# Kernel tuning notes

Measured on AMD Instinct MI355X. Metric: run time of the kernel, lower is better.

The kernel has to match this reference:

```python
import jax, jax.numpy as jnp
import numpy as np

NEG_BIG = -9.0e15  # matches torch's -9000000000000000.0
LEAKY_SLOPE = 0.01  # nn.LeakyReLU default


def setup_inputs() -> dict:
    key = jax.random.key(0)
    k1, k2, k3, k4, k5, k6 = jax.random.split(key, 6)
    B, N, NEMB, NHID = 1, 8192, 128, 64
    x = jax.random.normal(k1, (B, N, NEMB), dtype=jnp.float32)
    adj = jax.random.randint(k2, (B, N, N), 0, 2, dtype=jnp.int32)
    # learned parameters (xavier-ish scale)
    w_weight = jax.random.normal(k3, (NHID, NEMB), dtype=jnp.float32) * (1.0 / np.sqrt(NEMB))
    w_bias = jnp.zeros((NHID,), dtype=jnp.float32)
    a_weight = jax.random.normal(k4, (1, 2 * NHID), dtype=jnp.float32) * (1.0 / np.sqrt(2 * NHID))
    a_bias = jnp.zeros((1,), dtype=jnp.float32)
    return {"x": x, "adj": adj, "w_weight": w_weight, "w_bias": w_bias,
            "a_weight": a_weight, "a_bias": a_bias}


def reference(x, adj, w_weight, w_bias, a_weight, a_bias):
    # h = W x + b : [B, N, F]
    h = jnp.einsum("bnd,fd->bnf", x, w_weight) + w_bias
    F = h.shape[-1]
    # The torch code forms a[b,i,j] = concat(h_i, h_j) then Linear(2F->1).
    # Equivalent decomposition avoids the [B,N,N,2F] tensor:
    # e[b,i,j] = leaky_relu(h_i . a_src + h_j . a_dst + a_bias)
    a_src, a_dst = a_weight[0, :F], a_weight[0, F:]
    s_src = jnp.einsum("bnf,f->bn", h, a_src)  # [B, N]
    s_dst = jnp.einsum("bnf,f->bn", h, a_dst)  # [B, N]
    e = jax.nn.leaky_relu(s_src[:, :, None] + s_dst[:, None, :] + a_bias[0],
                          negative_slope=LEAKY_SLOPE)  # [B, N, N]
    # masked_scatter_ semantics: True positions (row-major over the WHOLE
    # flattened tensor) receive e's elements taken sequentially in order.
    mask_flat = (adj > 0).reshape(-1)
    take_idx = jnp.cumsum(mask_flat.astype(jnp.int32)) - 1  # position in source stream
    src_flat = e.reshape(-1)
    att = jnp.where(mask_flat, src_flat[take_idx], jnp.float32(NEG_BIG)).reshape(e.shape)
    # softmax over dim=2, dropout in eval mode (identity)
    att = jax.nn.softmax(att, axis=2)
    out = jax.nn.elu(jnp.einsum("bij,bjf->bif", att, h))  # [B, N, F]
    return out
```

## Files before the change

kernel.cpp:

```cpp
#include <hip/hip_runtime.h>
#include <cstdint>
#include <cstddef>

#define N 8192
#define F 64
#define NEMB 128
#define BI 16
#define BJ 256
#define NCHUNK 32
#define HALFCH 16
#define ROWSTR 560
#define LEAKY 0.01f
#define LOG2E 1.44269504f

typedef __attribute__((ext_vector_type(8))) short bf16x8;
typedef __attribute__((ext_vector_type(4))) float f32x4;

__device__ __forceinline__ float wave_reduce_sum_f(float v){
  #pragma unroll
  for (int d = 32; d > 0; d >>= 1) v += __shfl_xor(v, d, 64);
  return v;
}
__device__ __forceinline__ int wave_reduce_sum_i(int v){
  #pragma unroll
  for (int d = 32; d > 0; d >>= 1) v += __shfl_xor(v, d, 64);
  return v;
}
__device__ __forceinline__ int wave_incl_scan_i(int v, int lane){
  #pragma unroll
  for (int d = 1; d < 64; d <<= 1){
    int u = __shfl_up(v, d, 64);
    if (lane >= d) v += u;
  }
  return v;
}
__device__ __forceinline__ unsigned short f2bf(float x){
  union { float f; unsigned u; } v; v.f = x;
  unsigned r = v.u + 0x7fff + ((v.u >> 16) & 1);
  return (unsigned short)(r >> 16);
}

extern "C" __global__ void __launch_bounds__(256)
k_packh(const int* __restrict__ adj, unsigned short* __restrict__ bm,
        unsigned short* __restrict__ ccnt, int* __restrict__ rowtot,
        const float* __restrict__ x, const float* __restrict__ ww,
        const float* __restrict__ wb, const float* __restrict__ aw,
        const float* __restrict__ abias,
        float* __restrict__ h, float* __restrict__ ssrc, float* __restrict__ sdst2x){
  const int t = threadIdx.x;
  if (blockIdx.x < N){
    const int i = blockIdx.x;
    int total = 0;
    #pragma unroll
    for (int half = 0; half < 2; ++half){
      const int w = half*256 + t;
      const int4* p4 = (const int4*)(adj + (size_t)i*N + w*16);
      unsigned m = 0;
      #pragma unroll
      for (int k = 0; k < 4; ++k){
        int4 a = p4[k];
        m |= (unsigned)(a.x>0) << (k*4+0);
        m |= (unsigned)(a.y>0) << (k*4+1);
        m |= (unsigned)(a.z>0) << (k*4+2);
        m |= (unsigned)(a.w>0) << (k*4+3);
      }
      bm[((size_t)(i >> 4)*NCHUNK + (w >> 4))*256 + (i & 15)*16 + (w & 15)] =
          (unsigned short)m;
      const int pc = __popc(m);
      total += pc;
      int cs = pc;
      cs += __shfl_xor(cs, 1, 16);
      cs += __shfl_xor(cs, 2, 16);
      cs += __shfl_xor(cs, 4, 16);
      cs += __shfl_xor(cs, 8, 16);
      if ((t & 15) == 0) ccnt[(size_t)i*NCHUNK + (w>>4)] = (unsigned short)cs;
    }
    total = wave_reduce_sum_i(total);
    __shared__ int ws_[4];
    if ((t & 63) == 0) ws_[t >> 6] = total;
    __syncthreads();
    if (t == 0) rowtot[i] = ws_[0] + ws_[1] + ws_[2] + ws_[3];
  } else {
    const int w = t >> 6, lane = t & 63;
    __shared__ float xs[4][NEMB];
    const int n0 = (blockIdx.x - N) * 4;
    ((float2*)&xs[0][0])[t] = ((const float2*)(x + (size_t)n0 * NEMB))[t];
    __syncthreads();
    const int n = n0 + w;
    const float4* w4 = (const float4*)(ww + (size_t)lane * NEMB);
    const float4* x4 = (const float4*)&xs[w][0];
    float acc = wb[lane];
    #pragma unroll
    for (int k = 0; k < NEMB/4; ++k){
      float4 a = x4[k]; float4 b = w4[k];
      acc = fmaf(a.x, b.x, acc);
      acc = fmaf(a.y, b.y, acc);
      acc = fmaf(a.z, b.z, acc);
      acc = fmaf(a.w, b.w, acc);
    }
    h[(size_t)n * F + lane] = acc;
    float vs = wave_reduce_sum_f(acc * aw[lane]);
    float vd = wave_reduce_sum_f(acc * aw[F + lane]);
    if (lane == 0){
      ssrc[n] = (vs + abias[0]) * LOG2E;
      const float vdl = vd * LOG2E;
      sdst2x[n] = vdl; sdst2x[n + N] = vdl;
    }
  }
}

extern "C" __global__ void __launch_bounds__(256)
k_tr(const float* __restrict__ h, unsigned short* __restrict__ ht){
  __shared__ float tile[64][65];
  const int t = threadIdx.x;
  const int n0 = blockIdx.x * 64;
  #pragma unroll
  for (int s = 0; s < 4; ++s){
    const int r = s*16 + (t>>4);
    const int c = (t&15)*4;
    const float4 v = *(const float4*)(h + (size_t)(n0+r)*F + c);
    tile[r][c] = v.x; tile[r][c+1] = v.y; tile[r][c+2] = v.z; tile[r][c+3] = v.w;
  }
  __syncthreads();
  const int f = t >> 2, jq = t & 3;
  unsigned short buf[16];
  #pragma unroll
  for (int k = 0; k < 16; ++k) buf[k] = f2bf(tile[jq*16 + k][f]);
  *(uint4*)(ht + (size_t)f*N + n0 + jq*16)     = *(uint4*)&buf[0];
  *(uint4*)(ht + (size_t)f*N + n0 + jq*16 + 8) = *(uint4*)&buf[8];
}

extern "C" __global__ void __launch_bounds__(1024)
k_scan(const int* __restrict__ cnt, int* __restrict__ base){
  __shared__ int wsum[16];
  const int t = threadIdx.x, lane = t & 63, w = t >> 6;
  int4 aa = ((const int4*)cnt)[t * 2];
  int4 bb = ((const int4*)cnt)[t * 2 + 1];
  int v[8] = {aa.x, aa.y, aa.z, aa.w, bb.x, bb.y, bb.z, bb.w};
  int local = 0;
  #pragma unroll
  for (int k = 0; k < 8; ++k){ int tmp = v[k]; v[k] = local; local += tmp; }
  int inc = wave_incl_scan_i(local, lane);
  int wexcl = inc - local;
  if (lane == 63) wsum[w] = inc;
  __syncthreads();
  if (t == 0){
    int run = 0;
    #pragma unroll
    for (int k = 0; k < 16; ++k){ int tmp = wsum[k]; wsum[k] = run; run += tmp; }
  }
  __syncthreads();
  const int b0 = wsum[w] + wexcl;
  ((int4*)base)[t * 2]     = make_int4(b0 + v[0], b0 + v[1], b0 + v[2], b0 + v[3]);
  ((int4*)base)[t * 2 + 1] = make_int4(b0 + v[4], b0 + v[5], b0 + v[6], b0 + v[7]);
}

extern "C" __global__ void __launch_bounds__(256, 4)
k_main(const unsigned short* __restrict__ bm, const unsigned short* __restrict__ ccnt,
       const int* __restrict__ base, const unsigned short* __restrict__ ht,
       const float* __restrict__ ssrc, const float* __restrict__ sdst2x,
       float* __restrict__ pnum, float* __restrict__ pden){
  __shared__ __attribute__((aligned(16))) char pt[2][16*ROWSTR];
  __shared__ unsigned short ccum[BI][HALFCH];
  __shared__ int basel[BI];

  const int t = threadIdx.x, w = t >> 6, lane = t & 63;
  const int vid = blockIdx.x >> 1, half = blockIdx.x & 1;
  const int i0 = vid * BI;
  const int ch0 = half * HALFCH;

  if (t < BI) basel[t] = base[i0 + t];
  const int r = t >> 4, g = t & 15;
  {
    int c = (int)ccnt[(size_t)(i0+r)*NCHUNK + ch0 + g];
    int pre = 0;
    if (half){
      pre = (int)ccnt[(size_t)(i0+r)*NCHUNK + g];
      #pragma unroll
      for (int d = 1; d < 16; d <<= 1) pre += __shfl_xor(pre, d, 16);
    }
    int inc = c;
    #pragma unroll
    for (int d = 1; d < 16; d <<= 1){ int u = __shfl_up(inc, d, 16); if (g >= d) inc += u; }
    ccum[r][g] = (unsigned short)(pre + inc - c);
  }
  __syncthreads();

  const int fr = lane & 15, ks = lane >> 4;
  const int fB = w*16 + fr;
  char* buf0 = pt[0];
  char* buf1 = pt[1];
  const int rowbase = basel[r];
  float dsum = 0.f;
  f32x4 acc = {0.f, 0.f, 0.f, 0.f};
  bf16x8 bregA[8], bregB[8];

#define BMLD(CC) ((unsigned)bm[((size_t)vid*NCHUNK + ch0 + (CC))*256 + t])

#define PREFETCH(CH, BR) { \
    const unsigned short* hBp = ht + (size_t)fB*N + (CH)*BJ + ks*8; \
    _Pragma("unroll") \
    for (int kk = 0; kk < 8; ++kk) BR[kk] = *(const bf16x8*)(hBp + kk*32); \
    __builtin_amdgcn_sched_barrier(0); \
  }

#define PRODUCE(CC, PB, MV) { \
    const unsigned m = (MV); \
    const unsigned mlo = m & 0xffu, mhi = m >> 8; \
    const int clo = __popc(mlo), chi = __popc(mhi); \
    const int c = clo + chi; \
    int inc = c; \
    _Pragma("unroll") \
    for (int d = 1; d < 16; d <<= 1){ int u = __shfl_up(inc, d, 16); if (g >= d) inc += u; } \
    const int qex = inc - c; \
    const int q0row = rowbase + (int)ccum[r][CC]; \
    const float* sdw = sdst2x + (q0row & (N - 1)) + qex; \
    const int ilo = q0row >> 13; \
    const float s_lo = ssrc[ilo]; \
    const float s_hi = ssrc[ilo + 1]; \
    const int krel = ((ilo + 1) << 13) - q0row - qex; \
    char* myrow = (PB) + r*ROWSTR; \
    *(uint4*)(myrow + g*32)      = make_uint4(0,0,0,0); \
    *(uint4*)(myrow + g*32 + 16) = make_uint4(0,0,0,0); \
    float wvlo[8], wvhi[8]; \
    const float* sdh = sdw + clo; \
    _Pragma("unroll") \
    for (int k = 0; k < 8; ++k){ wvlo[k] = sdw[k]; wvhi[k] = sdh[k]; } \
    float dlo = 0.f, dhi = 0.f; \
    unsigned mcl = mlo, mch = mhi; \
    _Pragma("unroll") \
    for (int k = 0; k < 8; ++k){ \
      { \
        const float ss = (k >= krel) ? s_hi : s_lo; \
        float e = ss + wvlo[k]; \
        e = fmaxf(e, LEAKY * e); \
        float p; \
        asm("v_exp_f32 %0, %1" : "=v"(p) : "v"(e)); \
        const int pos = __ffs(mcl) - 1; \
        const bool act = (k < clo); \
        dlo += act ? p : 0.f; \
        const int off = act ? (g*32 + pos*2) : (512 + g*2); \
        *(unsigned short*)(myrow + off) = \
            (unsigned short)((__float_as_uint(p) + 0x8000u) >> 16); \
        mcl &= mcl - 1; \
      } \
      { \
        const int kg = clo + k; \
        const float ss = (kg >= krel) ? s_hi : s_lo; \
        float e = ss + wvhi[k]; \
        e = fmaxf(e, LEAKY * e); \
        float p; \
        asm("v_exp_f32 %0, %1" : "=v"(p) : "v"(e)); \
        const int pos = __ffs(mch) + 7; \
        const bool act = (k < chi); \
        dhi += act ? p : 0.f; \
        const int off = act ? (g*32 + pos*2) : (512 + g*2); \
        *(unsigned short*)(myrow + off) = \
            (unsigned short)((__float_as_uint(p) + 0x8000u) >> 16); \
        mch &= mch - 1; \
      } \
    } \
    dsum += dlo + dhi; \
  }

#define MM(PB, BR) { \
    const char* aP = (PB) + fr*ROWSTR; \
    __builtin_amdgcn_s_setprio(1); \
    _Pragma("unroll") \
    for (int kk = 0; kk < 8; ++kk){ \
      bf16x8 av = *(const bf16x8*)(aP + kk*64 + ks*16); \
      acc = __builtin_amdgcn_mfma_f32_16x16x32_bf16(av, BR[kk], acc, 0, 0, 0); \
    } \
    __builtin_amdgcn_s_setprio(0); \
  }

  unsigned mCur = BMLD(0);
  unsigned mNxt = BMLD(1);
  PREFETCH(ch0, bregA)
  PRODUCE(0, buf0, mCur)
  __syncthreads();
  for (int cc = 0; cc < HALFCH; cc += 2){
    {
      PREFETCH(ch0 + cc + 1, bregB)
      const unsigned mUse = mNxt;
      if (cc + 2 < HALFCH) mNxt = BMLD(cc + 2);
      PRODUCE(cc + 1, buf1, mUse)
      MM(buf0, bregA)
    }
    __syncthreads();
    if (cc + 2 < HALFCH){
      PREFETCH(ch0 + cc + 2, bregA)
      const unsigned mUse = mNxt;
      if (cc + 3 < HALFCH) mNxt = BMLD(cc + 3);
      PRODUCE(cc + 2, buf0, mUse)
      MM(buf1, bregB)
    } else {
      MM(buf1, bregB)
    }
    __syncthreads();
  }
#undef BMLD
#undef PREFETCH
#undef PRODUCE
#undef MM

  #pragma unroll
  for (int d = 8; d > 0; d >>= 1) dsum += __shfl_xor(dsum, d, 16);
  if (g == 0) pden[(size_t)half*N + i0 + r] = dsum;
  #pragma unroll
  for (int reg = 0; reg < 4; ++reg){
    const int il = ks*4 + reg;
    pnum[(size_t)half*N*F + (size_t)(i0 + il)*F + fB] = acc[reg];
  }
}

extern "C" __global__ void __launch_bounds__(256)
k_comb(const float* __restrict__ pnum, const float* __restrict__ pden,
       float* __restrict__ out){
  const int idx = blockIdx.x * 256 + threadIdx.x;
  const int i = idx >> 6;
  const float dn = pden[i] + pden[N + i];
  const float nm = pnum[idx] + pnum[(size_t)N*F + idx];
  float v = (dn > 0.f) ? nm / dn : 0.f;
  out[idx] = (v > 0.f) ? v : (__expf(v) - 1.f);
}

extern "C" void kernel_launch(void* const* d_in, const int* in_sizes, int n_in,
                              void* d_out, int out_size, void* d_ws, size_t ws_size,
                              hipStream_t stream){
  const float* x   = (const float*)d_in[0];
  const int*   adj = (const int*)d_in[1];
  const float* ww  = (const float*)d_in[2];
  const float* wb  = (const float*)d_in[3];
  const float* aw  = (const float*)d_in[4];
  const float* ab  = (const float*)d_in[5];
  float* out = (float*)d_out;

  char* ws = (char*)d_ws;
  float*          h      = (float*)(ws);
  unsigned short* ht     = (unsigned short*)(ws + (2u<<20));
  float*          ssrc   = (float*)(ws + (3u<<20));
  float*          sdst2x = (float*)(ws + (3u<<20) + 32*1024);
  int*            rowtot = (int*)(ws + (3u<<20) + 96*1024);
  int*            base   = (int*)(ws + (3u<<20) + 128*1024);
  unsigned short* ccnt   = (unsigned short*)(ws + (3u<<20) + 160*1024);
  unsigned short* bm     = (unsigned short*)(ws + (4u<<20));
  float*          pnum   = (float*)(ws + (12u<<20));
  float*          pden   = (float*)(ws + (16u<<20));

  k_packh<<<N + N/4, 256, 0, stream>>>(adj, bm, ccnt, rowtot,
                                       x, ww, wb, aw, ab, h, ssrc, sdst2x);
  k_tr  <<<N/64,   256, 0, stream>>>(h, ht);
  k_scan<<<1,     1024, 0, stream>>>(rowtot, base);
  k_main<<<2*(N/BI), 256, 0, stream>>>(bm, ccnt, base, ht, ssrc, sdst2x, pnum, pden);
  k_comb<<<(N*F)/256, 256, 0, stream>>>(pnum, pden, out);
}
```

Measured before the change: 160.5 us.

## Double column chunk width to 512 with 32-bit mask packing and single B register set

```diff
diff --git a/kernel.cpp b/kernel.cpp
--- a/kernel.cpp
+++ b/kernel.cpp
@@ -6,10 +6,10 @@
 #define F 64
 #define NEMB 128
 #define BI 16
-#define BJ 256
-#define NCHUNK 32
-#define HALFCH 16
-#define ROWSTR 560
+#define BJ 512
+#define NCH2 16
+#define HALFCH 8
+#define ROWSTR 1072
 #define LEAKY 0.01f
 #define LOG2E 1.44269504f
 
@@ -41,7 +41,7 @@
 }
 
 extern "C" __global__ void __launch_bounds__(256)
-k_packh(const int* __restrict__ adj, unsigned short* __restrict__ bm,
+k_packh(const int* __restrict__ adj, unsigned* __restrict__ bm32,
         unsigned short* __restrict__ ccnt, int* __restrict__ rowtot,
         const float* __restrict__ x, const float* __restrict__ ww,
         const float* __restrict__ wb, const float* __restrict__ aw,
@@ -64,16 +64,21 @@
         m |= (unsigned)(a.z>0) << (k*4+2);
         m |= (unsigned)(a.w>0) << (k*4+3);
       }
-      bm[((size_t)(i >> 4)*NCHUNK + (w >> 4))*256 + (i & 15)*16 + (w & 15)] =
-          (unsigned short)m;
+      const unsigned mo = (unsigned)__shfl_xor((int)m, 1, 64);
+      if ((t & 1) == 0){
+        const int w32 = w >> 1;
+        const int ch = w32 >> 4, gg = w32 & 15;
+        bm32[((size_t)(i >> 4)*NCH2 + ch)*256 + (i & 15)*16 + gg] = m | (mo << 16);
+      }
       const int pc = __popc(m);
       total += pc;
       int cs = pc;
-      cs += __shfl_xor(cs, 1, 16);
-      cs += __shfl_xor(cs, 2, 16);
-      cs += __shfl_xor(cs, 4, 16);
-      cs += __shfl_xor(cs, 8, 16);
-      if ((t & 15) == 0) ccnt[(size_t)i*NCHUNK + (w>>4)] = (unsigned short)cs;
+      cs += __shfl_xor(cs, 1, 32);
+      cs += __shfl_xor(cs, 2, 32);
+      cs += __shfl_xor(cs, 4, 32);
+      cs += __shfl_xor(cs, 8, 32);
+      cs += __shfl_xor(cs, 16, 32);
+      if ((t & 31) == 0) ccnt[(size_t)i*NCH2 + half*8 + (t>>5)] = (unsigned short)cs;
     }
     total = wave_reduce_sum_i(total);
     __shared__ int ws_[4];
@@ -156,7 +161,7 @@
 }
 
 extern "C" __global__ void __launch_bounds__(256, 4)
-k_main(const unsigned short* __restrict__ bm, const unsigned short* __restrict__ ccnt,
+k_main(const unsigned* __restrict__ bm32, const unsigned short* __restrict__ ccnt,
        const int* __restrict__ base, const unsigned short* __restrict__ ht,
        const float* __restrict__ ssrc, const float* __restrict__ sdst2x,
        float* __restrict__ pnum, float* __restrict__ pden){
@@ -172,17 +177,15 @@
   if (t < BI) basel[t] = base[i0 + t];
   const int r = t >> 4, g = t & 15;
   {
-    int c = (int)ccnt[(size_t)(i0+r)*NCHUNK + ch0 + g];
-    int pre = 0;
-    if (half){
-      pre = (int)ccnt[(size_t)(i0+r)*NCHUNK + g];
-      #pragma unroll
-      for (int d = 1; d < 16; d <<= 1) pre += __shfl_xor(pre, d, 16);
-    }
+    const unsigned short* cr = ccnt + (size_t)(i0+r)*NCH2;
+    int pre = (g < ch0) ? (int)cr[g] : 0;
+    #pragma unroll
+    for (int d = 1; d < 16; d <<= 1) pre += __shfl_xor(pre, d, 16);
+    int c = (g < HALFCH) ? (int)cr[ch0 + g] : 0;
     int inc = c;
     #pragma unroll
     for (int d = 1; d < 16; d <<= 1){ int u = __shfl_up(inc, d, 16); if (g >= d) inc += u; }
-    ccum[r][g] = (unsigned short)(pre + inc - c);
+    if (g < HALFCH) ccum[r][g] = (unsigned short)(pre + inc - c);
   }
   __syncthreads();
 
@@ -193,26 +196,47 @@
   const int rowbase = basel[r];
   float dsum = 0.f;
   f32x4 acc = {0.f, 0.f, 0.f, 0.f};
-  bf16x8 bregA[8], bregB[8];
-
-#define BMLD(CC) ((unsigned)bm[((size_t)vid*NCHUNK + ch0 + (CC))*256 + t])
-
-#define PREFETCH(CH, BR) { \
+  bf16x8 breg[16];
+
+#define BMLD(CC) (bm32[((size_t)vid*NCH2 + ch0 + (CC))*256 + t])
+
+#define PREFETCH(CH) { \
     const unsigned short* hBp = ht + (size_t)fB*N + (CH)*BJ + ks*8; \
     _Pragma("unroll") \
-    for (int kk = 0; kk < 8; ++kk) BR[kk] = *(const bf16x8*)(hBp + kk*32); \
+    for (int kk = 0; kk < 16; ++kk) breg[kk] = *(const bf16x8*)(hBp + kk*32); \
     __builtin_amdgcn_sched_barrier(0); \
   }
 
-#define PRODUCE(CC, PB, MV) { \
-    const unsigned m = (MV); \
-    const unsigned mlo = m & 0xffu, mhi = m >> 8; \
-    const int clo = __popc(mlo), chi = __popc(mhi); \
-    const int c = clo + chi; \
-    int inc = c; \
+#define CHAIN(MASK, CNT, WV, EOFF, BYOFF, DACC) \
+    { \
+      unsigned mc = (MASK); \
+      _Pragma("unroll") \
+      for (int k = 0; k < 8; ++k){ \
+        const int e = (EOFF) + k; \
+        const float ss = (e >= krel) ? s_hi : s_lo; \
+        float ev = ss + (WV)[k]; \
+        ev = fmaxf(ev, LEAKY * ev); \
+        float p; \
+        asm("v_exp_f32 %0, %1" : "=v"(p) : "v"(ev)); \
+        const int pos = __ffs(mc) - 1; \
+        const bool act = (k < (CNT)); \
+        DACC += act ? p : 0.f; \
+        const int off = act ? ((BYOFF) + pos*2) : (1024 + g*2); \
+        *(unsigned short*)(myrow + off) = \
+            (unsigned short)((__float_as_uint(p) + 0x8000u) >> 16); \
+        mc &= mc - 1; \
+      } \
+    }
+
+#define PRODUCE(CC, PB, UV) { \
+    const unsigned u_ = (UV); \
+    const unsigned mA = u_ & 0xffffu, mB = u_ >> 16; \
+    const int cA = __popc(mA), cB = __popc(mB); \
+    const int ct = cA + cB; \
+    int inc = ct; \
     _Pragma("unroll") \
-    for (int d = 1; d < 16; d <<= 1){ int u = __shfl_up(inc, d, 16); if (g >= d) inc += u; } \
-    const int qex = inc - c; \
+    for (int d = 1; d < 16; d <<= 1){ int uu = __shfl_up(inc, d, 16); if (g >= d) inc += uu; } \
+    const int qex = inc - ct; \
     const int q0row = rowbase + (int)ccum[r][CC]; \
     const float* sdw = sdst2x + (q0row & (N - 1)) + qex; \
     const int ilo = q0row >> 13; \
@@ -220,87 +244,65 @@
     const float s_hi = ssrc[ilo + 1]; \
     const int krel = ((ilo + 1) << 13) - q0row - qex; \
     char* myrow = (PB) + r*ROWSTR; \
-    *(uint4*)(myrow + g*32)      = make_uint4(0,0,0,0); \
-    *(uint4*)(myrow + g*32 + 16) = make_uint4(0,0,0,0); \
-    float wvlo[8], wvhi[8]; \
-    const float* sdh = sdw + clo; \
+    *(uint4*)(myrow + g*64)      = make_uint4(0,0,0,0); \
+    *(uint4*)(myrow + g*64 + 16) = make_uint4(0,0,0,0); \
+    *(uint4*)(myrow + g*64 + 32) = make_uint4(0,0,0,0); \
+    *(uint4*)(myrow + g*64 + 48) = make_uint4(0,0,0,0); \
+    const int cAlo = __popc(mA & 0xffu); \
+    const int cBlo = __popc(mB & 0xffu); \
+    float wv0[8], wv1[8], wv2[8], wv3[8]; \
+    const float* p1 = sdw + cAlo; \
+    const float* p2 = sdw + cA; \
+    const float* p3 = sdw + cA + cBlo; \
     _Pragma("unroll") \
-    for (int k = 0; k < 8; ++k){ wvlo[k] = sdw[k]; wvhi[k] = sdh[k]; } \
-    float dlo = 0.f, dhi = 0.f; \
-    unsigned mcl = mlo, mch = mhi; \
-    _Pragma("unroll") \
-    for (int k = 0; k < 8; ++k){ \
-      { \
-        const float ss = (k >= krel) ? s_hi : s_lo; \
-        float e = ss + wvlo[k]; \
-        e = fmaxf(e, LEAKY * e); \
-        float p; \
-        asm("v_exp_f32 %0, %1" : "=v"(p) : "v"(e)); \
-        const int pos = __ffs(mcl) - 1; \
-        const bool act = (k < clo); \
-        dlo += act ? p : 0.f; \
-        const int off = act ? (g*32 + pos*2) : (512 + g*2); \
-        *(unsigned short*)(myrow + off) = \
-            (unsigned short)((__float_as_uint(p) + 0x8000u) >> 16); \
-        mcl &= mcl - 1; \
-      } \
-      { \
-        const int kg = clo + k; \
-        const float ss = (kg >= krel) ? s_hi : s_lo; \
-        float e = ss + wvhi[k]; \
-        e = fmaxf(e, LEAKY * e); \
-        float p; \
-        asm("v_exp_f32 %0, %1" : "=v"(p) : "v"(e)); \
-        const int pos = __ffs(mch) + 7; \
-        const bool act = (k < chi); \
-        dhi += act ? p : 0.f; \
-        const int off = act ? (g*32 + pos*2) : (512 + g*2); \
-        *(unsigned short*)(myrow + off) = \
-            (unsigned short)((__float_as_uint(p) + 0x8000u) >> 16); \
-        mch &= mch - 1; \
-      } \
-    } \
-    dsum += dlo + dhi; \
-  }
-
-#define MM(PB, BR) { \
+    for (int k = 0; k < 8; ++k){ wv0[k] = sdw[k]; wv1[k] = p1[k]; wv2[k] = p2[k]; wv3[k] = p3[k]; } \
+    float d0 = 0.f, d1 = 0.f, d2 = 0.f, d3 = 0.f; \
+    CHAIN(mA & 0xffu, cAlo,      wv0, 0,           g*64,      d0) \
+    CHAIN(mA >> 8,    cA - cAlo, wv1, cAlo,        g*64 + 16, d1) \
+    CHAIN(mB & 0xffu, cBlo,      wv2, cA,          g*64 + 32, d2) \
+    CHAIN(mB >> 8,    cB - cBlo, wv3, cA + cBlo,   g*64 + 48, d3) \
+    dsum += (d0 + d1) + (d2 + d3); \
+  }
+
+#define MM(PB) { \
     const char* aP = (PB) + fr*ROWSTR; \
     __builtin_amdgcn_s_setprio(1); \
     _Pragma("unroll") \
-    for (int kk = 0; kk < 8; ++kk){ \
+    for (int kk = 0; kk < 16; ++kk){ \
       bf16x8 av = *(const bf16x8*)(aP + kk*64 + ks*16); \
-      acc = __builtin_amdgcn_mfma_f32_16x16x32_bf16(av, BR[kk], acc, 0, 0, 0); \
+      acc = __builtin_amdgcn_mfma_f32_16x16x32_bf16(av, breg[kk], acc, 0, 0, 0); \
     } \
     __builtin_amdgcn_s_setprio(0); \
   }
 
   unsigned mCur = BMLD(0);
   unsigned mNxt = BMLD(1);
-  PREFETCH(ch0, bregA)
+  PREFETCH(ch0)
   PRODUCE(0, buf0, mCur)
   __syncthreads();
   for (int cc = 0; cc < HALFCH; cc += 2){
     {
-      PREFETCH(ch0 + cc + 1, bregB)
       const unsigned mUse = mNxt;
       if (cc + 2 < HALFCH) mNxt = BMLD(cc + 2);
       PRODUCE(cc + 1, buf1, mUse)
-      MM(buf0, bregA)
+      MM(buf0)
+      PREFETCH(ch0 + cc + 1)
     }
     __syncthreads();
     if (cc + 2 < HALFCH){
-      PREFETCH(ch0 + cc + 2, bregA)
       const unsigned mUse = mNxt;
       if (cc + 3 < HALFCH) mNxt = BMLD(cc + 3);
       PRODUCE(cc + 2, buf0, mUse)
-      MM(buf1, bregB)
+      MM(buf1)
+      PREFETCH(ch0 + cc + 2)
     } else {
-      MM(buf1, bregB)
+      MM(buf1)
     }
     __syncthreads();
   }
 #undef BMLD
 #undef PREFETCH
+#undef CHAIN
 #undef PRODUCE
 #undef MM
 
@@ -344,14 +346,14 @@
   int*            rowtot = (int*)(ws + (3u<<20) + 96*1024);
   int*            base   = (int*)(ws + (3u<<20) + 128*1024);
   unsigned short* ccnt   = (unsigned short*)(ws + (3u<<20) + 160*1024);
-  unsigned short* bm     = (unsigned short*)(ws + (4u<<20));
+  unsigned*       bm32   = (unsigned*)(ws + (4u<<20));
   float*          pnum   = (float*)(ws + (12u<<20));
   float*          pden   = (float*)(ws + (16u<<20));
 
-  k_packh<<<N + N/4, 256, 0, stream>>>(adj, bm, ccnt, rowtot,
+  k_packh<<<N + N/4, 256, 0, stream>>>(adj, bm32, ccnt, rowtot,
                                        x, ww, wb, aw, ab, h, ssrc, sdst2x);
   k_tr  <<<N/64,   256, 0, stream>>>(h, ht);
   k_scan<<<1,     1024, 0, stream>>>(rowtot, base);
-  k_main<<<2*(N/BI), 256, 0, stream>>>(bm, ccnt, base, ht, ssrc, sdst2x, pnum, pden);
+  k_main<<<2*(N/BI), 256, 0, stream>>>(bm32, ccnt, base, ht, ssrc, sdst2x, pnum, pden);
   k_comb<<<(N*F)/256, 256, 0, stream>>>(pnum, pden, out);
 }
```

Result: slower. 192.0 us (+19.6%).
